# Kernel tuning notes

Hardware: AMD Instinct MI355X
Metric: run time of the kernel (lower is better)

## Reference

```python
import jax, jax.numpy as jnp
import numpy as np

# Model dims (match init_kwargs)
D_MODEL = 1024
D_INNER = 2048
D_STATE = 16
D_CONV = 4
DT_RANK = 64
H = 8                      # num_heads
P = D_INNER // H           # head_dim = 256
DT_MIN, DT_MAX = 1e-4, 1.0
BATCH, SEQ = 2, 4096
TOTAL_OUT = 2 * D_INNER + DT_RANK + 2 * H * D_STATE  # 4416 (no gated delta)
EPS = 1e-6


def _xavier(k, shape):
    fan_out, fan_in = shape
    return jax.random.normal(k, shape, jnp.float32) * np.sqrt(2.0 / (fan_in + fan_out))


def setup_inputs() -> dict:
    key = jax.random.key(0)
    ks = jax.random.split(key, 8)
    x = jax.random.normal(ks[0], (BATCH, SEQ, D_MODEL), jnp.float32)
    W_in = _xavier(ks[1], (TOTAL_OUT, D_MODEL))          # in_proj (no bias)
    W_dt = _xavier(ks[2], (H, DT_RANK))                  # dt_proj (no bias)
    conv_w = jax.random.normal(ks[3], (D_INNER, D_CONV), jnp.float32) * 0.1
    conv_b = jnp.zeros((D_INNER,), jnp.float32)
    # A_log init: log(1..d_state) per head
    A_log = jnp.broadcast_to(jnp.log(jnp.arange(1, D_STATE + 1, dtype=jnp.float32)), (H, D_STATE))
    Dskip = jnp.ones((H, P), jnp.float32)
    # dt_bias = inverse_softplus(dt), dt log-uniform in [dt_min, dt_max]
    dt0 = jnp.exp(jax.random.uniform(ks[4], (H,), jnp.float32)
                  * (np.log(DT_MAX) - np.log(DT_MIN)) + np.log(DT_MIN))
    dt_bias = dt0 + jnp.log(-jnp.expm1(-dt0))
    norm_w = jnp.ones((D_INNER,), jnp.float32)
    W_out = _xavier(ks[5], (D_MODEL, D_INNER))
    W_res = _xavier(ks[6], (D_INNER, D_MODEL))           # residual_proj (d_model != d_inner)
    return dict(x=x, W_in=W_in, W_dt=W_dt, conv_w=conv_w, conv_b=conv_b,
                A_log=A_log, Dskip=Dskip, dt_bias=dt_bias, norm_w=norm_w,
                W_out=W_out, W_res=W_res)


def _causal_dwconv(u, w, b):
    # u: (B,L,C) -> causal depthwise conv along L. w: (C,K), b: (C,)
    lhs = u.transpose(0, 2, 1)               # (B,C,L)
    rhs = w[:, None, :]                      # (C,1,K)
    out = jax.lax.conv_general_dilated(
        lhs, rhs, window_strides=(1,), padding=[(D_CONV - 1, 0)],
        dimension_numbers=('NCH', 'OIH', 'NCH'), feature_group_count=D_INNER)
    return (out + b[None, :, None]).transpose(0, 2, 1)


def reference(x, W_in, W_dt, conv_w, conv_b, A_log, Dskip, dt_bias, norm_w, W_out, W_res):
    Bsz, L, _ = x.shape
    p = x @ W_in.T                                            # (B,L,TOTAL_OUT)
    splits = np.cumsum([D_INNER, D_INNER, DT_RANK, H * D_STATE]).tolist()
    z, u, dt_h, Bf, Cf = jnp.split(p, splits, axis=-1)
    Bp = Bf.reshape(Bsz, L, H, D_STATE)
    Cp = Cf.reshape(Bsz, L, H, D_STATE)
    u = _causal_dwconv(u, conv_w, conv_b)                     # (B,L,D_INNER)
    # dt_prep: softplus(dt_raw + bias) clamped to [dt_min, dt_max]
    dt = jnp.clip(jax.nn.softplus(dt_h @ W_dt.T + dt_bias), DT_MIN, DT_MAX)  # (B,L,H)
    A = -jnp.exp(A_log)                                       # (H,N)
    uh = u.reshape(Bsz, L, H, P)

    def step(h, inp):
        u_t, dt_t, B_t, C_t = inp                             # (B,H,P),(B,H),(B,H,N),(B,H,N)
        dA = jnp.exp(dt_t[..., None] * A)                     # (B,H,N)
        h = h * dA[:, :, None, :] + (dt_t[:, :, None, None] * u_t[..., None]) * B_t[:, :, None, :]
        y_t = jnp.einsum('bhpn,bhn->bhp', h, C_t)
        return h, y_t

    h0 = jnp.zeros((Bsz, H, P, D_STATE), x.dtype)
    xs = (uh.transpose(1, 0, 2, 3), dt.transpose(1, 0, 2),
          Bp.transpose(1, 0, 2, 3), Cp.transpose(1, 0, 2, 3))
    _, ys = jax.lax.scan(step, h0, xs)                        # (L,B,H,P)
    y = ys.transpose(1, 0, 2, 3) + Dskip[None, None] * uh     # skip connection
    y = y.reshape(Bsz, L, D_INNER)

    residual_inner = x @ W_res.T                              # residual_proj
    # fused_out: g = RMSNorm(y * silu(z) + residual) * weight
    g = y * jax.nn.silu(z) + residual_inner
    g = g * jax.lax.rsqrt(jnp.mean(g * g, axis=-1, keepdims=True) + EPS) * norm_w
    return g @ W_out.T
```

## Files before the change

kernel.cpp:

```cpp
#include <hip/hip_runtime.h>
#include <hip/hip_bf16.h>
#include <math.h>

#define DMODEL  1024
#define DINNER  2048
#define DSTATE  16
#define DCONV   4
#define DTRANK  64
#define NH      8
#define PH      256
#define TOTOUT  4416
#define NTOT2   6528
#define MB_ROWS 4096
#define LC      64
#define NCB     (MB_ROWS/LC)

typedef __attribute__((ext_vector_type(8))) short bf16x8;
typedef __attribute__((ext_vector_type(4))) float f32x4;

__device__ inline unsigned cvt2bf(float lo, float hi) {
    unsigned r;
    asm("v_cvt_pk_bf16_f32 %0, %1, %2" : "=v"(r) : "v"(lo), "v"(hi));
    return r;
}
__device__ inline ushort f2bf(float v) { return (ushort)(cvt2bf(v, v) & 0xffffu); }
__device__ inline float bf2f(ushort u) {
    union { unsigned u; float f; } w; w.u = (unsigned)u << 16; return w.f;
}
__device__ inline void gload16(const ushort* g, ushort* l) {
    __builtin_amdgcn_global_load_lds((const __attribute__((address_space(1))) unsigned*)(const void*)g,
                                     (__attribute__((address_space(3))) unsigned*)(void*)l, 16, 0, 0);
}

__global__ __launch_bounds__(256) void cvt_all(const float* __restrict__ W_in,
                                               const float* __restrict__ W_res,
                                               const float* __restrict__ W_out,
                                               const float* __restrict__ x,
                                               ushort* __restrict__ WB,
                                               ushort* __restrict__ XBF) {
    const size_t E_WCAT = (size_t)NTOT2 * DMODEL;
    const size_t E_WOUT = E_WCAT + (size_t)DMODEL * DINNER;
    size_t i = ((size_t)blockIdx.x * 256 + threadIdx.x) * 8;
    const float* src;
    ushort* dst;
    bool zero = false;
    if (i < E_WCAT) {
        size_t r = i >> 10, c = i & 1023;
        if (r < 4096)       src = W_in + (r << 10) + c;
        else if (r < 6144)  src = W_res + ((r - 4096) << 10) + c;
        else if (r < 6464)  src = W_in + ((r - 2048) << 10) + c;
        else { src = W_in; zero = true; }
        dst = WB + i;
    } else if (i < E_WOUT) {
        src = W_out + (i - E_WCAT);
        dst = WB + i;
    } else {
        src = x + (i - E_WOUT);
        dst = XBF + (i - E_WOUT);
    }
    float4 v0, v1;
    if (zero) { v0 = make_float4(0.f, 0.f, 0.f, 0.f); v1 = v0; }
    else { v0 = *(const float4*)src; v1 = *(const float4*)(src + 4); }
    uint4 o;
    o.x = cvt2bf(v0.x, v0.y); o.y = cvt2bf(v0.z, v0.w);
    o.z = cvt2bf(v1.x, v1.y); o.w = cvt2bf(v1.z, v1.w);
    *(uint4*)dst = o;
}

__global__ __launch_bounds__(512) void gemm_fused(const ushort* __restrict__ A,
                                                  const ushort* __restrict__ W,
                                                  ushort* __restrict__ Zb,
                                                  ushort* __restrict__ Ub,
                                                  ushort* __restrict__ RESb,
                                                  float* __restrict__ DBCp,
                                                  int ntx, int K) {
    __shared__ __align__(16) ushort L[3 * 12288];
    const int nwg  = gridDim.x;
    const int orig = blockIdx.x;
    const int swz  = (orig & 7) * (nwg >> 3) + (orig >> 3);
    const int bx = swz % ntx, by = swz / ntx;
    const int row0 = by * 256, col0 = bx * 128;

    const int t    = threadIdx.x;
    const int lane = t & 63, w = t >> 6;
    const int wr   = w >> 1, wc = w & 1;
    const int l15  = lane & 15, l4 = lane >> 4;

    const int r0g = t >> 2, s0g = t & 3;
    const int r1g = r0g + 128;
    const int rr0 = r0g ^ ((r0g >> 3) & 1), cc0 = s0g ^ ((r0g >> 1) & 3);
    const int rr1 = r1g ^ ((r1g >> 3) & 1), cc1 = s0g ^ ((r1g >> 1) & 3);
    const ushort* sA0 = A + (size_t)(row0 + rr0) * K + cc0 * 8;
    const ushort* sA1 = A + (size_t)(row0 + rr1) * K + cc1 * 8;
    const ushort* sB0 = W + (size_t)(col0 + rr0) * K + cc0 * 8;

    int offA[4], offB[4];
    #pragma unroll
    for (int mi = 0; mi < 4; mi++) {
        int rq = wr * 64 + mi * 16 + l15;
        offA[mi] = (rq * 32 + l4 * 8) ^ (((rq >> 1) & 7) << 3);
    }
    #pragma unroll
    for (int ni = 0; ni < 4; ni++) {
        int rq = wc * 64 + ni * 16 + l15;
        offB[ni] = 8192 + ((rq * 32 + l4 * 8) ^ (((rq >> 1) & 7) << 3));
    }

    f32x4 acc[4][4];
    #pragma unroll
    for (int i = 0; i < 4; i++)
        #pragma unroll
        for (int j = 0; j < 4; j++)
            acc[i][j] = (f32x4){0.f, 0.f, 0.f, 0.f};

    const int KT = K >> 5;
    gload16(sA0,      &L[t * 8]);
    gload16(sA1,      &L[4096 + t * 8]);
    gload16(sB0,      &L[8192 + t * 8]);
    gload16(sA0 + 32, &L[12288 + t * 8]);
    gload16(sA1 + 32, &L[12288 + 4096 + t * 8]);
    gload16(sB0 + 32, &L[12288 + 8192 + t * 8]);
    asm volatile("s_waitcnt vmcnt(3)" ::: "memory");
    __builtin_amdgcn_sched_barrier(0);
    __builtin_amdgcn_s_barrier();
    __builtin_amdgcn_sched_barrier(0);

    for (int kt = 0; kt < KT; ++kt) {
        const bool pre = (kt + 2) < KT;
        if (pre) {
            ushort* bp2 = &L[((kt + 2) % 3) * 12288];
            const int ko = (kt + 2) << 5;
            gload16(sA0 + ko, bp2 + t * 8);
            gload16(sA1 + ko, bp2 + 4096 + t * 8);
            gload16(sB0 + ko, bp2 + 8192 + t * 8);
        }
        const ushort* bp = &L[(kt % 3) * 12288];
        bf16x8 af[4], bw[4];
        #pragma unroll
        for (int mi = 0; mi < 4; mi++) af[mi] = *(const bf16x8*)(bp + offA[mi]);
        #pragma unroll
        for (int ni = 0; ni < 4; ni++) bw[ni] = *(const bf16x8*)(bp + offB[ni]);
        __builtin_amdgcn_s_setprio(1);
        #pragma unroll
        for (int mi = 0; mi < 4; mi++)
            #pragma unroll
            for (int ni = 0; ni < 4; ni++)
                acc[mi][ni] = __builtin_amdgcn_mfma_f32_16x16x32_bf16(af[mi], bw[ni], acc[mi][ni], 0, 0, 0);
        __builtin_amdgcn_s_setprio(0);
        if (pre) { asm volatile("s_waitcnt vmcnt(3)" ::: "memory"); }
        else     { asm volatile("s_waitcnt vmcnt(0)" ::: "memory"); }
        __builtin_amdgcn_sched_barrier(0);
        __builtin_amdgcn_s_barrier();
        __builtin_amdgcn_sched_barrier(0);
    }

    #pragma unroll
    for (int mi = 0; mi < 4; mi++) {
        #pragma unroll
        for (int ni = 0; ni < 4; ni++) {
            #pragma unroll
            for (int rr = 0; rr < 4; rr++) {
                const int row = row0 + wr * 64 + mi * 16 + l4 * 4 + rr;
                const int col = col0 + wc * 64 + ni * 16 + l15;
                const float v = acc[mi][ni][rr];
                if (col0 < DINNER) {
                    Zb[(size_t)row * DINNER + col] = f2bf(v);
                } else if (col0 < 2 * DINNER) {
                    Ub[(size_t)row * DINNER + (col - DINNER)] = f2bf(v);
                } else if (col0 < 3 * DINNER) {
                    RESb[(size_t)row * DINNER + (col - 2 * DINNER)] = f2bf(v);
                } else {
                    if (col < 3 * DINNER + 320)
                        DBCp[(size_t)row * 320 + (col - 3 * DINNER)] = v;
                }
            }
        }
    }
}

__global__ __launch_bounds__(256) void gemm_out128(const ushort* __restrict__ A,
                                                   const ushort* __restrict__ W,
                                                   float* __restrict__ C0,
                                                   int ntx, int K, int ldc) {
    __shared__ __align__(16) ushort L[3 * 8192];
    const int nwg  = gridDim.x;
    const int orig = blockIdx.x;
    const int swz  = (orig & 7) * (nwg >> 3) + (orig >> 3);
    const int bx = swz % ntx, by = swz / ntx;
    const int row0 = by * 128, col0 = bx * 128;

    const int t    = threadIdx.x;
    const int lane = t & 63, w = t >> 6;
    const int wr   = w >> 1, wc = w & 1;
    const int l15  = lane & 15, l4 = lane >> 4;

    const int r0g = t >> 2, s0g = t & 3;
    const int r1g = r0g + 64;
    const int rr0 = r0g ^ ((r0g >> 3) & 1), cc0 = s0g ^ ((r0g >> 1) & 3);
    const int rr1 = r1g ^ ((r1g >> 3) & 1), cc1 = s0g ^ ((r1g >> 1) & 3);
    const ushort* sA0 = A + (size_t)(row0 + rr0) * K + cc0 * 8;
    const ushort* sA1 = A + (size_t)(row0 + rr1) * K + cc1 * 8;
    const ushort* sB0 = W + (size_t)(col0 + rr0) * K + cc0 * 8;
    const ushort* sB1 = W + (size_t)(col0 + rr1) * K + cc1 * 8;

    int offA[4], offB[4];
    #pragma unroll
    for (int mi = 0; mi < 4; mi++) {
        int rq = wr * 64 + mi * 16 + l15;
        offA[mi] = (rq * 32 + l4 * 8) ^ (((rq >> 1) & 7) << 3);
    }
    #pragma unroll
    for (int ni = 0; ni < 4; ni++) {
        int rq = wc * 64 + ni * 16 + l15;
        offB[ni] = 4096 + ((rq * 32 + l4 * 8) ^ (((rq >> 1) & 7) << 3));
    }

    f32x4 acc[4][4];
    #pragma unroll
    for (int i = 0; i < 4; i++)
        #pragma unroll
        for (int j = 0; j < 4; j++)
            acc[i][j] = (f32x4){0.f, 0.f, 0.f, 0.f};

    const int KT = K >> 5;
    gload16(sA0,      &L[t * 8]);
    gload16(sA1,      &L[2048 + t * 8]);
    gload16(sB0,      &L[4096 + t * 8]);
    gload16(sB1,      &L[6144 + t * 8]);
    gload16(sA0 + 32, &L[8192 + t * 8]);
    gload16(sA1 + 32, &L[8192 + 2048 + t * 8]);
    gload16(sB0 + 32, &L[8192 + 4096 + t * 8]);
    gload16(sB1 + 32, &L[8192 + 6144 + t * 8]);
    asm volatile("s_waitcnt vmcnt(4)" ::: "memory");
    __builtin_amdgcn_sched_barrier(0);
    __builtin_amdgcn_s_barrier();
    __builtin_amdgcn_sched_barrier(0);

    for (int kt = 0; kt < KT; ++kt) {
        const bool pre = (kt + 2) < KT;
        if (pre) {
            ushort* bp2 = &L[((kt + 2) % 3) * 8192];
            const int ko = (kt + 2) << 5;
            gload16(sA0 + ko, bp2 + t * 8);
            gload16(sA1 + ko, bp2 + 2048 + t * 8);
            gload16(sB0 + ko, bp2 + 4096 + t * 8);
            gload16(sB1 + ko, bp2 + 6144 + t * 8);
        }
        const ushort* bp = &L[(kt % 3) * 8192];
        bf16x8 af[4], bw[4];
        #pragma unroll
        for (int mi = 0; mi < 4; mi++) af[mi] = *(const bf16x8*)(bp + offA[mi]);
        #pragma unroll
        for (int ni = 0; ni < 4; ni++) bw[ni] = *(const bf16x8*)(bp + offB[ni]);
        __builtin_amdgcn_s_setprio(1);
        #pragma unroll
        for (int mi = 0; mi < 4; mi++)
            #pragma unroll
            for (int ni = 0; ni < 4; ni++)
                acc[mi][ni] = __builtin_amdgcn_mfma_f32_16x16x32_bf16(af[mi], bw[ni], acc[mi][ni], 0, 0, 0);
        __builtin_amdgcn_s_setprio(0);
        if (pre) { asm volatile("s_waitcnt vmcnt(4)" ::: "memory"); }
        else     { asm volatile("s_waitcnt vmcnt(0)" ::: "memory"); }
        __builtin_amdgcn_sched_barrier(0);
        __builtin_amdgcn_s_barrier();
        __builtin_amdgcn_sched_barrier(0);
    }

    #pragma unroll
    for (int mi = 0; mi < 4; mi++)
        #pragma unroll
        for (int ni = 0; ni < 4; ni++)
            #pragma unroll
            for (int rr = 0; rr < 4; rr++) {
                const int row = row0 + wr * 64 + mi * 16 + l4 * 4 + rr;
                const int col = col0 + wc * 64 + ni * 16 + l15;
                C0[(size_t)row * ldc + col] = acc[mi][ni][rr];
            }
}

__global__ __launch_bounds__(256) void scan_local(const ushort* __restrict__ Ub,
                                                  const float* __restrict__ DBC,
                                                  const float* __restrict__ W_dt,
                                                  const float* __restrict__ dt_bias,
                                                  const float* __restrict__ A_log,
                                                  const float* __restrict__ cw,
                                                  const float* __restrict__ cb,
                                                  float* __restrict__ hloc,
                                                  float* __restrict__ Pc) {
    const int c = blockIdx.x, h = blockIdx.y;
    const int pidx = threadIdx.x;
    const int ch = h * PH + pidx;
    const int t0 = c * LC;
    __shared__ float sdt[LC];
    __shared__ float sdA[LC][DSTATE];
    __shared__ float sdB[LC][DSTATE];
    const int st = pidx >> 4, sn = pidx & 15;

    if (pidx < LC) {
        const float* row = DBC + (size_t)(t0 + pidx) * 320;
        const float* wd = W_dt + h * DTRANK;
        float acc = dt_bias[h];
        #pragma unroll 16
        for (int r2 = 0; r2 < DTRANK; r2++) acc = fmaf(row[r2], wd[r2], acc);
        float sp = acc > 20.f ? acc : log1pf(expf(acc));
        sdt[pidx] = fminf(fmaxf(sp, 1e-4f), 1.0f);
    }
    const float w0 = cw[ch * 4], w1 = cw[ch * 4 + 1], w2 = cw[ch * 4 + 2], w3 = cw[ch * 4 + 3];
    const float bia = cb[ch];
    const int bs = (c / NCB) * MB_ROWS;
    float um3 = (t0 - 3 >= bs) ? bf2f(Ub[(size_t)(t0 - 3) * DINNER + ch]) : 0.f;
    float um2 = (t0 - 2 >= bs) ? bf2f(Ub[(size_t)(t0 - 2) * DINNER + ch]) : 0.f;
    float um1 = (t0 - 1 >= bs) ? bf2f(Ub[(size_t)(t0 - 1) * DINNER + ch]) : 0.f;
    __syncthreads();

    {
        const float nA = -expf(A_log[h * DSTATE + sn]);
        #pragma unroll
        for (int j = 0; j < 4; j++) {
            int tt = st + j * 16;
            size_t trow = (size_t)(t0 + tt);
            float dv = sdt[tt];
            sdA[tt][sn] = expf(dv * nA);
            sdB[tt][sn] = dv * DBC[trow * 320 + 64 + h * DSTATE + sn];
        }
    }
    __syncthreads();

    float hst[DSTATE] = {};
    for (int t = 0; t < LC; t++) {
        float u0 = bf2f(Ub[(size_t)(t0 + t) * DINNER + ch]);
        float up = fmaf(w3, u0, fmaf(w2, um1, fmaf(w1, um2, fmaf(w0, um3, bia))));
        um3 = um2; um2 = um1; um1 = u0;
        #pragma unroll
        for (int n = 0; n < DSTATE; n++)
            hst[n] = fmaf(hst[n], sdA[t][n], up * sdB[t][n]);
    }
    float* hl = hloc + (((size_t)c * NH + h) * PH + pidx) * DSTATE;
    #pragma unroll
    for (int n = 0; n < DSTATE; n++) hl[n] = hst[n];

    if (pidx < DSTATE) {
        float pr = 1.f;
        for (int t = 0; t < LC; t++) pr *= sdA[t][pidx];
        Pc[((size_t)c * NH + h) * DSTATE + pidx] = pr;
    }
}

__global__ __launch_bounds__(256) void scan_carry(const float* __restrict__ hloc,
                                                  const float* __restrict__ Pc,
                                                  float* __restrict__ Hent) {
    int g = blockIdx.x * 256 + threadIdx.x;
    int b = g >> 15;
    int r = g & 32767;
    int h = r >> 12;
    int inner = r & 4095;
    int n = r & 15;
    float carry = 0.f;
    for (int i = 0; i < NCB; i++) {
        int c = b * NCB + i;
        size_t idx = ((size_t)c * NH + h) * (PH * DSTATE) + inner;
        Hent[idx] = carry;
        carry = fmaf(Pc[((size_t)c * NH + h) * DSTATE + n], carry, hloc[idx]);
    }
}

__global__ __launch_bounds__(256) void scan_out(const ushort* __restrict__ Zb,
                                                const ushort* __restrict__ Ub,
                                                const ushort* __restrict__ RESb,
                                                ushort* __restrict__ Yb,
                                                const float* __restrict__ DBC,
                                                const float* __restrict__ W_dt,
                                                const float* __restrict__ dt_bias,
                                                const float* __restrict__ A_log,
                                                const float* __restrict__ cw,
                                                const float* __restrict__ cb,
                                                const float* __restrict__ Dskip,
                                                const float* __restrict__ Hent) {
    const int c = blockIdx.x, h = blockIdx.y;
    const int pidx = threadIdx.x;
    const int ch = h * PH + pidx;
    const int t0 = c * LC;
    __shared__ float sdt[LC];
    __shared__ float sdA[LC][DSTATE];
    __shared__ float sdB[LC][DSTATE];
    __shared__ float sC [LC][DSTATE];
    const int st = pidx >> 4, sn = pidx & 15;

    if (pidx < LC) {
        const float* row = DBC + (size_t)(t0 + pidx) * 320;
        const float* wd = W_dt + h * DTRANK;
        float acc = dt_bias[h];
        #pragma unroll 16
        for (int r2 = 0; r2 < DTRANK; r2++) acc = fmaf(row[r2], wd[r2], acc);
        float sp = acc > 20.f ? acc : log1pf(expf(acc));
        sdt[pidx] = fminf(fmaxf(sp, 1e-4f), 1.0f);
    }
    const float w0 = cw[ch * 4], w1 = cw[ch * 4 + 1], w2 = cw[ch * 4 + 2], w3 = cw[ch * 4 + 3];
    const float bia = cb[ch];
    const int bs = (c / NCB) * MB_ROWS;
    float um3 = (t0 - 3 >= bs) ? bf2f(Ub[(size_t)(t0 - 3) * DINNER + ch]) : 0.f;
    float um2 = (t0 - 2 >= bs) ? bf2f(Ub[(size_t)(t0 - 2) * DINNER + ch]) : 0.f;
    float um1 = (t0 - 1 >= bs) ? bf2f(Ub[(size_t)(t0 - 1) * DINNER + ch]) : 0.f;
    __syncthreads();

    {
        const float nA = -expf(A_log[h * DSTATE + sn]);
        #pragma unroll
        for (int j = 0; j < 4; j++) {
            int tt = st + j * 16;
            size_t trow = (size_t)(t0 + tt);
            float dv = sdt[tt];
            sdA[tt][sn] = expf(dv * nA);
            sdB[tt][sn] = dv * DBC[trow * 320 + 64 + h * DSTATE + sn];
            sC [tt][sn] =      DBC[trow * 320 + 192 + h * DSTATE + sn];
        }
    }
    const float dsk = Dskip[ch];
    float hst[DSTATE];
    const float* he = Hent + (((size_t)c * NH + h) * PH + pidx) * DSTATE;
    #pragma unroll
    for (int n = 0; n < DSTATE; n++) hst[n] = he[n];
    __syncthreads();

    for (int t = 0; t < LC; t++) {
        size_t off = (size_t)(t0 + t) * DINNER + ch;
        float u0 = bf2f(Ub[off]);
        float up = fmaf(w3, u0, fmaf(w2, um1, fmaf(w1, um2, fmaf(w0, um3, bia))));
        um3 = um2; um2 = um1; um1 = u0;
        float a0 = 0.f, a1 = 0.f, a2 = 0.f, a3 = 0.f;
        #pragma unroll
        for (int n = 0; n < 4; n++) {
            hst[n +  0] = fmaf(hst[n +  0], sdA[t][n +  0], up * sdB[t][n +  0]);
            hst[n +  4] = fmaf(hst[n +  4], sdA[t][n +  4], up * sdB[t][n +  4]);
            hst[n +  8] = fmaf(hst[n +  8], sdA[t][n +  8], up * sdB[t][n +  8]);
            hst[n + 12] = fmaf(hst[n + 12], sdA[t][n + 12], up * sdB[t][n + 12]);
            a0 = fmaf(hst[n +  0], sC[t][n +  0], a0);
            a1 = fmaf(hst[n +  4], sC[t][n +  4], a1);
            a2 = fmaf(hst[n +  8], sC[t][n +  8], a2);
            a3 = fmaf(hst[n + 12], sC[t][n + 12], a3);
        }
        float yv = ((a0 + a1) + (a2 + a3)) + dsk * up;
        float zv = bf2f(Zb[off]);
        float sil = zv / (1.f + expf(-zv));
        Yb[off] = f2bf(fmaf(yv, sil, bf2f(RESb[off])));
    }
}

__global__ __launch_bounds__(256) void rmsnorm_bf(const ushort* __restrict__ Yb,
                                                  const float* __restrict__ norm_w,
                                                  ushort* __restrict__ Gb) {
    const int row = blockIdx.x;
    const ushort* r = Yb + (size_t)row * DINNER;
    const int c0 = threadIdx.x * 8;
    uint4 packed = *(const uint4*)(r + c0);
    float v[8];
    v[0] = bf2f((ushort)(packed.x & 0xffff)); v[1] = bf2f((ushort)(packed.x >> 16));
    v[2] = bf2f((ushort)(packed.y & 0xffff)); v[3] = bf2f((ushort)(packed.y >> 16));
    v[4] = bf2f((ushort)(packed.z & 0xffff)); v[5] = bf2f((ushort)(packed.z >> 16));
    v[6] = bf2f((ushort)(packed.w & 0xffff)); v[7] = bf2f((ushort)(packed.w >> 16));
    float ss = 0.f;
    #pragma unroll
    for (int i = 0; i < 8; i++) ss = fmaf(v[i], v[i], ss);
    #pragma unroll
    for (int off = 32; off > 0; off >>= 1) ss += __shfl_down(ss, off);
    __shared__ float red[4];
    if ((threadIdx.x & 63) == 0) red[threadIdx.x >> 6] = ss;
    __syncthreads();
    float tot = red[0] + red[1] + red[2] + red[3];
    float inv = rsqrtf(tot / (float)DINNER + 1e-6f);
    float4 w0 = *(const float4*)(norm_w + c0);
    float4 w1 = *(const float4*)(norm_w + c0 + 4);
    uint4 o;
    o.x = cvt2bf(v[0] * inv * w0.x, v[1] * inv * w0.y);
    o.y = cvt2bf(v[2] * inv * w0.z, v[3] * inv * w0.w);
    o.z = cvt2bf(v[4] * inv * w1.x, v[5] * inv * w1.y);
    o.w = cvt2bf(v[6] * inv * w1.z, v[7] * inv * w1.w);
    *(uint4*)(Gb + (size_t)row * DINNER + c0) = o;
}

struct Lay {
    float *DBC, *PC, *HLOC, *HENT;
    ushort *YB, *ZB, *UB, *RESB, *XBF, *WB;
    size_t total;
};
static Lay mk_layout(char* base, int Mr) {
    size_t o = 0;
    auto take = [&](size_t bytes) { char* p = base + o; o = (o + bytes + 255) & ~(size_t)255; return p; };
    Lay l;
    l.YB   = (ushort*)take((size_t)Mr * 2048 * 2);
    l.DBC  = (float*) take((size_t)Mr * 320 * 4);
    l.PC   = (float*) take((size_t)(Mr / 64) * NH * DSTATE * 4);
    l.HLOC = (float*) take((size_t)Mr * 512 * 4);
    l.HENT = (float*) take((size_t)Mr * 512 * 4);
    l.ZB   = (ushort*)take((size_t)Mr * 2048 * 2);
    l.UB   = (ushort*)take((size_t)Mr * 2048 * 2);
    l.RESB = (ushort*)take((size_t)Mr * 2048 * 2);
    l.XBF  = (ushort*)take((size_t)8192 * 1024 * 2);
    l.WB   = (ushort*)take(((size_t)NTOT2 * 1024 + (size_t)1024 * 2048) * 2);
    l.total = o;
    return l;
}

extern "C" void kernel_launch(void* const* d_in, const int* in_sizes, int n_in,
                              void* d_out, int out_size, void* d_ws, size_t ws_size,
                              hipStream_t stream) {
    const float* x       = (const float*)d_in[0];
    const float* W_in    = (const float*)d_in[1];
    const float* W_dt    = (const float*)d_in[2];
    const float* conv_w  = (const float*)d_in[3];
    const float* conv_b  = (const float*)d_in[4];
    const float* A_log   = (const float*)d_in[5];
    const float* Dskip   = (const float*)d_in[6];
    const float* dt_bias = (const float*)d_in[7];
    const float* norm_w  = (const float*)d_in[8];
    const float* W_out   = (const float*)d_in[9];
    const float* W_res   = (const float*)d_in[10];
    float* out = (float*)d_out;

    Lay probe = mk_layout(nullptr, 2 * MB_ROWS);
    const bool fat = ws_size >= probe.total;
    const int Mr = fat ? 2 * MB_ROWS : MB_ROWS;
    const int npass = fat ? 1 : 2;
    const int nbc = fat ? 2 : 1;
    Lay l = mk_layout((char*)d_ws, Mr);

    ushort* wcat = l.WB;
    ushort* wotb = wcat + (size_t)NTOT2 * 1024;
    ushort* Gb   = l.ZB;

    {
        const size_t total_gran = ((size_t)NTOT2 * 1024 + (size_t)1024 * 2048 + (size_t)8192 * 1024) / 8;
        cvt_all<<<(int)(total_gran / 256), 256, 0, stream>>>(W_in, W_res, W_out, x, l.WB, l.XBF);
    }

    for (int b = 0; b < npass; b++) {
        const ushort* xb = l.XBF + (size_t)b * MB_ROWS * DMODEL;
        float* outb = out + (size_t)b * MB_ROWS * DMODEL;

        gemm_fused<<<51 * (Mr / 256), 512, 0, stream>>>(xb, wcat, l.ZB, l.UB, l.RESB, l.DBC, 51, DMODEL);
        scan_local<<<dim3(Mr / LC, NH), 256, 0, stream>>>(l.UB, l.DBC, W_dt, dt_bias, A_log,
                                                          conv_w, conv_b, l.HLOC, l.PC);
        scan_carry<<<nbc * 128, 256, 0, stream>>>(l.HLOC, l.PC, l.HENT);
        scan_out<<<dim3(Mr / LC, NH), 256, 0, stream>>>(l.ZB, l.UB, l.RESB, l.YB, l.DBC,
                                                        W_dt, dt_bias, A_log,
                                                        conv_w, conv_b, Dskip, l.HENT);
        rmsnorm_bf<<<Mr, 256, 0, stream>>>(l.YB, norm_w, Gb);
        gemm_out128<<<8 * (Mr / 128), 256, 0, stream>>>(Gb, wotb, outb, 8, DINNER, DMODEL);
    }
}
```

Measured before the change: 297.2 us.

## Fuse RMSNorm into scan output and out-projection epilogue

Removes the separate RMSNorm kernel. scan_out now also computes per-head partial sums of squares for each row. The norm weight is folded into the bf16 W_out conversion, and the out GEMM epilogue applies the per-row rsqrt scale. This drops one full read and write pass over the 2048-wide activation plus a kernel launch. In exchange it adds a small partial-sum buffer, and the sum of squares is now taken from fp32 values instead of bf16-rounded ones.

```diff
diff --git a/kernel.cpp b/kernel.cpp
--- a/kernel.cpp
+++ b/kernel.cpp
@@ -35,6 +35,7 @@
 __global__ __launch_bounds__(256) void cvt_all(const float* __restrict__ W_in,
                                                const float* __restrict__ W_res,
                                                const float* __restrict__ W_out,
+                                               const float* __restrict__ norm_w,
                                                const float* __restrict__ x,
                                                ushort* __restrict__ WB,
                                                ushort* __restrict__ XBF) {
@@ -43,7 +44,8 @@
     size_t i = ((size_t)blockIdx.x * 256 + threadIdx.x) * 8;
     const float* src;
     ushort* dst;
-    bool zero = false;
+    bool zero = false, scale = false;
+    size_t k0 = 0;
     if (i < E_WCAT) {
         size_t r = i >> 10, c = i & 1023;
         if (r < 4096)       src = W_in + (r << 10) + c;
@@ -52,8 +54,11 @@
         else { src = W_in; zero = true; }
         dst = WB + i;
     } else if (i < E_WOUT) {
-        src = W_out + (i - E_WCAT);
+        size_t o = i - E_WCAT;
+        src = W_out + o;
         dst = WB + i;
+        scale = true;
+        k0 = o & (DINNER - 1);
     } else {
         src = x + (i - E_WOUT);
         dst = XBF + (i - E_WOUT);
@@ -61,6 +66,12 @@
     float4 v0, v1;
     if (zero) { v0 = make_float4(0.f, 0.f, 0.f, 0.f); v1 = v0; }
     else { v0 = *(const float4*)src; v1 = *(const float4*)(src + 4); }
+    if (scale) {
+        float4 n0 = *(const float4*)(norm_w + k0);
+        float4 n1 = *(const float4*)(norm_w + k0 + 4);
+        v0.x *= n0.x; v0.y *= n0.y; v0.z *= n0.z; v0.w *= n0.w;
+        v1.x *= n1.x; v1.y *= n1.y; v1.z *= n1.z; v1.w *= n1.w;
+    }
     uint4 o;
     o.x = cvt2bf(v0.x, v0.y); o.y = cvt2bf(v0.z, v0.w);
     o.z = cvt2bf(v1.x, v1.y); o.w = cvt2bf(v1.z, v1.w);
@@ -180,6 +191,7 @@
 
 __global__ __launch_bounds__(256) void gemm_out128(const ushort* __restrict__ A,
                                                    const ushort* __restrict__ W,
+                                                   const float* __restrict__ ssqp,
                                                    float* __restrict__ C0,
                                                    int ntx, int K, int ldc) {
     __shared__ __align__(16) ushort L[3 * 8192];
@@ -266,6 +278,17 @@
         __builtin_amdgcn_sched_barrier(0);
     }
 
+    float inv[4][4];
+    #pragma unroll
+    for (int mi = 0; mi < 4; mi++)
+        #pragma unroll
+        for (int rr = 0; rr < 4; rr++) {
+            const int row = row0 + wr * 64 + mi * 16 + l4 * 4 + rr;
+            const float* p = ssqp + (size_t)row * 8;
+            float s = ((p[0] + p[1]) + (p[2] + p[3])) + ((p[4] + p[5]) + (p[6] + p[7]));
+            inv[mi][rr] = rsqrtf(s * (1.f / (float)DINNER) + 1e-6f);
+        }
+
     #pragma unroll
     for (int mi = 0; mi < 4; mi++)
         #pragma unroll
@@ -274,7 +297,7 @@
             for (int rr = 0; rr < 4; rr++) {
                 const int row = row0 + wr * 64 + mi * 16 + l4 * 4 + rr;
                 const int col = col0 + wc * 64 + ni * 16 + l15;
-                C0[(size_t)row * ldc + col] = acc[mi][ni][rr];
+                C0[(size_t)row * ldc + col] = acc[mi][ni][rr] * inv[mi][rr];
             }
 }
 
@@ -368,6 +391,7 @@
                                                 const ushort* __restrict__ Ub,
                                                 const ushort* __restrict__ RESb,
                                                 ushort* __restrict__ Yb,
+                                                float* __restrict__ ssqp,
                                                 const float* __restrict__ DBC,
                                                 const float* __restrict__ W_dt,
                                                 const float* __restrict__ dt_bias,
@@ -380,10 +404,12 @@
     const int pidx = threadIdx.x;
     const int ch = h * PH + pidx;
     const int t0 = c * LC;
+    const int wv = pidx >> 6, lane = pidx & 63;
     __shared__ float sdt[LC];
     __shared__ float sdA[LC][DSTATE];
     __shared__ float sdB[LC][DSTATE];
     __shared__ float sC [LC][DSTATE];
+    __shared__ float sred[LC][4];
     const int st = pidx >> 4, sn = pidx & 15;
 
     if (pidx < LC) {
@@ -442,44 +468,22 @@
         float yv = ((a0 + a1) + (a2 + a3)) + dsk * up;
         float zv = bf2f(Zb[off]);
         float sil = zv / (1.f + expf(-zv));
-        Yb[off] = f2bf(fmaf(yv, sil, bf2f(RESb[off])));
-    }
-}
-
-__global__ __launch_bounds__(256) void rmsnorm_bf(const ushort* __restrict__ Yb,
-                                                  const float* __restrict__ norm_w,
-                                                  ushort* __restrict__ Gb) {
-    const int row = blockIdx.x;
-    const ushort* r = Yb + (size_t)row * DINNER;
-    const int c0 = threadIdx.x * 8;
-    uint4 packed = *(const uint4*)(r + c0);
-    float v[8];
-    v[0] = bf2f((ushort)(packed.x & 0xffff)); v[1] = bf2f((ushort)(packed.x >> 16));
-    v[2] = bf2f((ushort)(packed.y & 0xffff)); v[3] = bf2f((ushort)(packed.y >> 16));
-    v[4] = bf2f((ushort)(packed.z & 0xffff)); v[5] = bf2f((ushort)(packed.z >> 16));
-    v[6] = bf2f((ushort)(packed.w & 0xffff)); v[7] = bf2f((ushort)(packed.w >> 16));
-    float ss = 0.f;
-    #pragma unroll
-    for (int i = 0; i < 8; i++) ss = fmaf(v[i], v[i], ss);
-    #pragma unroll
-    for (int off = 32; off > 0; off >>= 1) ss += __shfl_down(ss, off);
-    __shared__ float red[4];
-    if ((threadIdx.x & 63) == 0) red[threadIdx.x >> 6] = ss;
+        float gv = fmaf(yv, sil, bf2f(RESb[off]));
+        Yb[off] = f2bf(gv);
+        float ss = gv * gv;
+        #pragma unroll
+        for (int o2 = 32; o2 > 0; o2 >>= 1) ss += __shfl_down(ss, o2);
+        if (lane == 0) sred[t][wv] = ss;
+    }
     __syncthreads();
-    float tot = red[0] + red[1] + red[2] + red[3];
-    float inv = rsqrtf(tot / (float)DINNER + 1e-6f);
-    float4 w0 = *(const float4*)(norm_w + c0);
-    float4 w1 = *(const float4*)(norm_w + c0 + 4);
-    uint4 o;
-    o.x = cvt2bf(v[0] * inv * w0.x, v[1] * inv * w0.y);
-    o.y = cvt2bf(v[2] * inv * w0.z, v[3] * inv * w0.w);
-    o.z = cvt2bf(v[4] * inv * w1.x, v[5] * inv * w1.y);
-    o.w = cvt2bf(v[6] * inv * w1.z, v[7] * inv * w1.w);
-    *(uint4*)(Gb + (size_t)row * DINNER + c0) = o;
+    if (pidx < LC) {
+        float s4 = (sred[pidx][0] + sred[pidx][1]) + (sred[pidx][2] + sred[pidx][3]);
+        ssqp[(size_t)(t0 + pidx) * 8 + h] = s4;
+    }
 }
 
 struct Lay {
-    float *DBC, *PC, *HLOC, *HENT;
+    float *DBC, *PC, *HLOC, *HENT, *SSQP;
     ushort *YB, *ZB, *UB, *RESB, *XBF, *WB;
     size_t total;
 };
@@ -492,6 +496,7 @@
     l.PC   = (float*) take((size_t)(Mr / 64) * NH * DSTATE * 4);
     l.HLOC = (float*) take((size_t)Mr * 512 * 4);
     l.HENT = (float*) take((size_t)Mr * 512 * 4);
+    l.SSQP = (float*) take((size_t)Mr * 8 * 4);
     l.ZB   = (ushort*)take((size_t)Mr * 2048 * 2);
     l.UB   = (ushort*)take((size_t)Mr * 2048 * 2);
     l.RESB = (ushort*)take((size_t)Mr * 2048 * 2);
@@ -526,11 +531,10 @@
 
     ushort* wcat = l.WB;
     ushort* wotb = wcat + (size_t)NTOT2 * 1024;
-    ushort* Gb   = l.ZB;
 
     {
         const size_t total_gran = ((size_t)NTOT2 * 1024 + (size_t)1024 * 2048 + (size_t)8192 * 1024) / 8;
-        cvt_all<<<(int)(total_gran / 256), 256, 0, stream>>>(W_in, W_res, W_out, x, l.WB, l.XBF);
+        cvt_all<<<(int)(total_gran / 256), 256, 0, stream>>>(W_in, W_res, W_out, norm_w, x, l.WB, l.XBF);
     }
 
     for (int b = 0; b < npass; b++) {
@@ -541,10 +545,9 @@
         scan_local<<<dim3(Mr / LC, NH), 256, 0, stream>>>(l.UB, l.DBC, W_dt, dt_bias, A_log,
                                                           conv_w, conv_b, l.HLOC, l.PC);
         scan_carry<<<nbc * 128, 256, 0, stream>>>(l.HLOC, l.PC, l.HENT);
-        scan_out<<<dim3(Mr / LC, NH), 256, 0, stream>>>(l.ZB, l.UB, l.RESB, l.YB, l.DBC,
+        scan_out<<<dim3(Mr / LC, NH), 256, 0, stream>>>(l.ZB, l.UB, l.RESB, l.YB, l.SSQP, l.DBC,
                                                         W_dt, dt_bias, A_log,
                                                         conv_w, conv_b, Dskip, l.HENT);
-        rmsnorm_bf<<<Mr, 256, 0, stream>>>(l.YB, norm_w, Gb);
-        gemm_out128<<<8 * (Mr / 128), 256, 0, stream>>>(Gb, wotb, outb, 8, DINNER, DMODEL);
-    }
-}
+        gemm_out128<<<8 * (Mr / 128), 256, 0, stream>>>(l.YB, wotb, l.SSQP, outb, 8, DINNER, DMODEL);
+    }
+}
```

New measurement: 298.0 us. No clear change (+0.3%).
